# Kernel tuning notes

Measured on AMD Instinct MI355X. Metric: run time of the kernel, lower is better.

Reference implementation:

```python
import jax, jax.numpy as jnp
import numpy as np

DIAG = 4  # number of distinct power-of-2 diagonal bands; must divide H


def _diag_mask(H, L):
    # head h in group g = h // (H // DIAG) uses tril diagonal offset 2**g - 1.
    # True entries are MASKED (filled with -inf), except the last key column
    # which is always kept (cur_mask[:, -1] = 0 in the torch code).
    group = H // DIAG
    offs = 2 ** (jnp.arange(H) // group) - 1            # [H]
    rows = jnp.arange(L)[:, None]                        # [L,1] query index
    cols = jnp.arange(L)[None, :]                        # [1,L] key index
    mask = (cols <= rows + offs[:, None, None]) & (cols != L - 1)  # [H,L,L]
    return mask


def setup_inputs() -> dict:
    key = jax.random.key(0)
    kq, kk, kv = jax.random.split(key, 3)
    B, L, H, E = 4, 2048, 16, 64
    queries = jax.random.normal(kq, (B, L, H, E), dtype=jnp.float32)
    keys = jax.random.normal(kk, (B, L, H, E), dtype=jnp.float32)
    values = jax.random.normal(kv, (B, L, H, E), dtype=jnp.float32)
    return {"queries": queries, "keys": keys, "values": values}


def reference(queries, keys, values):
    B, L, H, E = queries.shape
    scale = 1.0 / np.sqrt(E).astype(np.float32)
    # [B,H,L,S]
    scores = jnp.einsum('blhe,bshe->bhls', queries, keys)
    mask = _diag_mask(H, L)                              # [H,L,L]
    scores = jnp.where(mask[None], -jnp.inf, scores)
    A = jax.nn.softmax(scale * scores, axis=-1)          # dropout inactive (eval)
    V = jnp.einsum('bhls,bshd->blhd', A, values)
    return V
```

## Files before the change

### kernel.cpp

```cpp
#include <hip/hip_runtime.h>
#include <stdint.h>

using f32x4  = __attribute__((ext_vector_type(4))) float;
using f32x16 = __attribute__((ext_vector_type(16))) float;
using s16x8  = __attribute__((ext_vector_type(8))) short;
using u16x4  = __attribute__((ext_vector_type(4))) unsigned short;
using u32x4  = __attribute__((ext_vector_type(4))) unsigned int;

typedef __attribute__((address_space(3))) unsigned int lds_u32;
typedef __attribute__((address_space(1))) unsigned int glb_u32;

__device__ __forceinline__ unsigned short f2bf(float f){
  union { float f; unsigned u; } x; x.f = f;
  return (unsigned short)((x.u + 0x7FFFu + ((x.u >> 16) & 1u)) >> 16);
}
__device__ __forceinline__ unsigned cvt_pk(float lo, float hi){
  unsigned r;
  asm("v_cvt_pk_bf16_f32 %0, %1, %2" : "=v"(r) : "v"(lo), "v"(hi));
  return r;
}
__device__ __forceinline__ void plswap(unsigned &a, unsigned &b){
  asm volatile("v_permlane32_swap_b32 %0, %1" : "+v"(a), "+v"(b));
}

#if __has_builtin(__builtin_amdgcn_exp2f)
#define EXP2F(x) __builtin_amdgcn_exp2f(x)
#else
#define EXP2F(x) exp2f(x)
#endif

#define MFMA16(A,B,C) __builtin_amdgcn_mfma_f32_16x16x32_bf16((A),(B),(C),0,0,0)
#define MFMA32(A,B,C) __builtin_amdgcn_mfma_f32_32x32x16_bf16((A),(B),(C),0,0,0)

constexpr int   L      = 2048;
constexpr int   H      = 16;
constexpr int   E      = 64;
constexpr int   HE     = 1024;
constexpr float SCALE  = 0.125f;
constexpr float QSCALE = 0.18033688011112042f;

__global__ __launch_bounds__(256)
void prep_kv(const float* __restrict__ Kg, const float* __restrict__ Vg,
             unsigned short* __restrict__ Ko, unsigned short* __restrict__ Vo){
  __shared__ __align__(16) unsigned short t8[4096];
  const int g0 = blockIdx.x;
  const int t  = threadIdx.x;
  if (g0 < 2048){
    const int gid = g0;
    const int jt = gid & 31, bh = gid >> 5;
    const int b = bh >> 4, h = bh & 15;
    const int key6 = t >> 2;
    const int p    = t & 3;
    const int kb = key6 >> 5, k31 = key6 & 31;
    const float* src = Kg + ((size_t)((b*2048 + jt*64 + key6)*16 + h) << 6) + p*16;
    const float4 v0 = *reinterpret_cast<const float4*>(src);
    const float4 v1 = *reinterpret_cast<const float4*>(src + 4);
    const float4 v2 = *reinterpret_cast<const float4*>(src + 8);
    const float4 v3 = *reinterpret_cast<const float4*>(src + 12);
    s16x8 f0, f1;
    f0[0]=(short)f2bf(v0.x); f0[1]=(short)f2bf(v0.y); f0[2]=(short)f2bf(v0.z); f0[3]=(short)f2bf(v0.w);
    f0[4]=(short)f2bf(v1.x); f0[5]=(short)f2bf(v1.y); f0[6]=(short)f2bf(v1.z); f0[7]=(short)f2bf(v1.w);
    f1[0]=(short)f2bf(v2.x); f1[1]=(short)f2bf(v2.y); f1[2]=(short)f2bf(v2.z); f1[3]=(short)f2bf(v2.w);
    f1[4]=(short)f2bf(v3.x); f1[5]=(short)f2bf(v3.y); f1[6]=(short)f2bf(v3.z); f1[7]=(short)f2bf(v3.w);
    const int slot0 = ((kb*4 + p)*2 + 0)*32 + k31;
    *reinterpret_cast<s16x8*>(&t8[slot0*8])      = f0;
    *reinterpret_cast<s16x8*>(&t8[(slot0+32)*8]) = f1;
    __syncthreads();
    unsigned short* dst = Ko + ((size_t)gid << 12) + t*16;
    *reinterpret_cast<s16x8*>(dst)     = *reinterpret_cast<const s16x8*>(&t8[t*16]);
    *reinterpret_cast<s16x8*>(dst + 8) = *reinterpret_cast<const s16x8*>(&t8[t*16 + 8]);
  } else {
    const int gid = g0 - 2048;
    const int jt = gid & 31, bh = gid >> 5;
    const int b = bh >> 4, h = bh & 15;
    const int key6 = t >> 2;
    const int p    = t & 3;
    const int kc = key6 >> 4, h2 = (key6 >> 3) & 1, kr = key6 & 7;
    const float* src = Vg + ((size_t)((b*2048 + jt*64 + key6)*16 + h) << 6) + p*16;
    float vv[16];
    #pragma unroll
    for (int q = 0; q < 4; ++q){
      const float4 v = *reinterpret_cast<const float4*>(src + q*4);
      vv[q*4+0]=v.x; vv[q*4+1]=v.y; vv[q*4+2]=v.z; vv[q*4+3]=v.w;
    }
    #pragma unroll
    for (int j = 0; j < 16; ++j){
      const int e  = p*16 + j;
      const int eb = e >> 5, e31 = e & 31;
      const int slot = ((eb*4 + kc)*2 + h2)*32 + e31;
      t8[slot*8 + kr] = f2bf(vv[j]);
    }
    __syncthreads();
    unsigned short* dst = Vo + ((size_t)gid << 12) + t*16;
    *reinterpret_cast<s16x8*>(dst)     = *reinterpret_cast<const s16x8*>(&t8[t*16]);
    *reinterpret_cast<s16x8*>(dst + 8) = *reinterpret_cast<const s16x8*>(&t8[t*16 + 8]);
  }
}

__global__ __launch_bounds__(512, 4)
void attn13(const float* __restrict__ Qg, const unsigned short* __restrict__ Kbg,
            const unsigned short* __restrict__ Vtg, float* __restrict__ Og)
{
  __shared__ __align__(16) unsigned short Kbuf[2][4096];
  __shared__ __align__(16) unsigned short Vbuf[2][4096];

  const int tid  = threadIdx.x;
  const int wave = tid >> 6;
  const int lane = tid & 63;
  const int c    = lane & 31;
  const int hi   = lane >> 5;

  const int gid = blockIdx.x;
  const int u   = gid >> 6;
  const int bh  = gid & 63;
  const int qb  = (u < 4) ? u : (11 - u);
  const int b = bh >> 4, h = bh & 15;
  const int off = (1 << (h >> 2)) - 1;

  const int    qrow0 = 256 * qb + wave * 32;
  const size_t fbase = (size_t)b * L * HE + (size_t)h * 64;
  const size_t tbase = (size_t)bh * 32;

  s16x8 qf[4];
  {
    const float* qp_ = Qg + fbase + (size_t)(qrow0 + c) * HE;
    #pragma unroll
    for (int ec = 0; ec < 4; ++ec){
      const float4 a  = *reinterpret_cast<const float4*>(qp_ + ec*16 + hi*8);
      const float4 b2 = *reinterpret_cast<const float4*>(qp_ + ec*16 + hi*8 + 4);
      s16x8 v;
      v[0]=(short)f2bf(a.x*QSCALE);  v[1]=(short)f2bf(a.y*QSCALE);
      v[2]=(short)f2bf(a.z*QSCALE);  v[3]=(short)f2bf(a.w*QSCALE);
      v[4]=(short)f2bf(b2.x*QSCALE); v[5]=(short)f2bf(b2.y*QSCALE);
      v[6]=(short)f2bf(b2.z*QSCALE); v[7]=(short)f2bf(b2.w*QSCALE);
      qf[ec] = v;
    }
  }

  s16x8 ones;
  #pragma unroll
  for (int j = 0; j < 8; ++j) ones[j] = (short)0x3F80;

  f32x16 acc0, acc1, accl;
  #pragma unroll
  for (int r = 0; r < 16; ++r){ acc0[r]=0.f; acc1[r]=0.f; accl[r]=0.f; }

  const int j0   = 4 * qb;
  const int qlim = qrow0 + c + off;

  auto STAGE = [&](int jt, int nb){
    const unsigned short* gk = Kbg + ((size_t)(tbase + jt) << 12) + (size_t)(wave*512 + lane*8);
    const unsigned short* gv = Vtg + ((size_t)(tbase + jt) << 12) + (size_t)(wave*512 + lane*8);
    __builtin_amdgcn_global_load_lds((const glb_u32*)gk,
        (lds_u32*)&Kbuf[nb][wave*512], 16, 0, 0);
    __builtin_amdgcn_global_load_lds((const glb_u32*)gv,
        (lds_u32*)&Vbuf[nb][wave*512], 16, 0, 0);
  };

  auto COMP = [&](int jt, int nb){
    const int s0 = jt * 64;
    if ((jt < 31) && (s0 + 63 <= qrow0 + off)) return;
    const unsigned short* KB = Kbuf[nb];
    const unsigned short* VB = Vbuf[nb];

    f32x16 S0, S1;
    #pragma unroll
    for (int r = 0; r < 16; ++r){ S0[r]=0.f; S1[r]=0.f; }
    __builtin_amdgcn_s_setprio(1);
    #pragma unroll
    for (int ec = 0; ec < 4; ++ec){
      const s16x8 k0 = *reinterpret_cast<const s16x8*>(&KB[(((0*4+ec)*2+hi)*32 + c)*8]);
      const s16x8 k1 = *reinterpret_cast<const s16x8*>(&KB[(((1*4+ec)*2+hi)*32 + c)*8]);
      S0 = MFMA32(k0, qf[ec], S0);
      S1 = MFMA32(k1, qf[ec], S1);
    }
    __builtin_amdgcn_s_setprio(0);

    if ((jt == 31) || (s0 <= qrow0 + 31 + off)){
      #pragma unroll
      for (int r = 0; r < 16; ++r){
        const int kg0 = s0 + (r&3) + 8*(r>>2) + 4*hi;
        const int kg1 = kg0 + 32;
        if (!((kg0 > qlim) || (kg0 == L-1))) S0[r] = -1e30f;
        if (!((kg1 > qlim) || (kg1 == L-1))) S1[r] = -1e30f;
      }
    }

    #pragma unroll
    for (int r = 0; r < 16; ++r){
      S0[r] = EXP2F(S0[r]);
      S1[r] = EXP2F(S1[r]);
    }

    __builtin_amdgcn_s_setprio(1);
    #define PV_STEP(Pv, kh, kcg) { \
      unsigned a0 = cvt_pk(Pv[8*(kh)+0], Pv[8*(kh)+1]); \
      unsigned a1 = cvt_pk(Pv[8*(kh)+2], Pv[8*(kh)+3]); \
      unsigned b0 = cvt_pk(Pv[8*(kh)+4], Pv[8*(kh)+5]); \
      unsigned b1 = cvt_pk(Pv[8*(kh)+6], Pv[8*(kh)+7]); \
      plswap(a0, b0); plswap(a1, b1); \
      u32x4 afu; afu[0]=a0; afu[1]=a1; afu[2]=b0; afu[3]=b1; \
      const s16x8 af = __builtin_bit_cast(s16x8, afu); \
      const s16x8 vf0 = *reinterpret_cast<const s16x8*>(&VB[(((0*4+(kcg))*2+hi)*32 + c)*8]); \
      const s16x8 vf1 = *reinterpret_cast<const s16x8*>(&VB[(((1*4+(kcg))*2+hi)*32 + c)*8]); \
      acc0 = MFMA32(af, vf0, acc0); \
      acc1 = MFMA32(af, vf1, acc1); \
      accl = MFMA32(af, ones, accl); \
    }
    PV_STEP(S0, 0, 0)
    PV_STEP(S0, 1, 1)
    PV_STEP(S1, 0, 2)
    PV_STEP(S1, 1, 3)
    #undef PV_STEP
    __builtin_amdgcn_s_setprio(0);
  };

  #define WAITBAR2 asm volatile("s_waitcnt vmcnt(2)\n\ts_barrier" ::: "memory")
  #define WAITBAR0 asm volatile("s_waitcnt vmcnt(0)\n\ts_barrier" ::: "memory")
  #define BARRIER  __builtin_amdgcn_s_barrier()

  STAGE(j0, 0);
  STAGE(j0 + 1, 1);

  for (int jt = j0; jt < 30; ++jt){
    WAITBAR2;
    COMP(jt, jt & 1);
    BARRIER;
    STAGE(jt + 2, jt & 1);
  }
  WAITBAR2;
  COMP(30, 0);
  WAITBAR0;
  COMP(31, 1);

  #undef WAITBAR2
  #undef WAITBAR0
  #undef BARRIER

  #pragma unroll
  for (int r = 0; r < 16; ++r){
    const int rowr = (r&3) + 8*(r>>2) + 4*hi;
    const float li = 1.0f / accl[r];
    float* op = Og + fbase + (size_t)(qrow0 + rowr) * HE;
    op[c]      = acc0[r] * li;
    op[32 + c] = acc1[r] * li;
  }
}

__global__ __launch_bounds__(512)
void attn_band(const float* __restrict__ Qg, const float* __restrict__ Kg,
               const float* __restrict__ Vg, float* __restrict__ Og)
{
  __shared__ __align__(16) unsigned short Ks[64*64];
  __shared__ __align__(16) unsigned short Vs[64*64];
  __shared__ __align__(16) unsigned short Ps[8][16*64];
  const int tid  = threadIdx.x;
  const int wave = tid >> 6;
  const int lane = tid & 63;
  const int lo16 = lane & 15;
  const int hi4  = lane >> 4;
  const int gid = blockIdx.x;
  const int qb  = gid & 15;
  const int bh  = gid >> 4;
  const int b   = bh >> 4;
  const int h   = bh & 15;
  const int off = (1 << (h >> 2)) - 1;
  const int    r0   = qb * 128;
  const size_t base = (size_t)b * L * HE + (size_t)h * 64;
  const int qrow0 = r0 + wave * 16;
  s16x8 qf[2];
  {
    const float* qp = Qg + base + (size_t)(qrow0 + lo16) * HE;
    #pragma unroll
    for (int ec = 0; ec < 2; ++ec){
      const int e0 = ec*32 + hi4*8;
      s16x8 v;
      #pragma unroll
      for (int j = 0; j < 8; ++j) v[j] = (short)f2bf(qp[e0 + j]);
      qf[ec] = v;
    }
  }
  f32x4 acc[4];
  #pragma unroll
  for (int et = 0; et < 4; ++et) acc[et] = f32x4{0.f,0.f,0.f,0.f};
  float m_run[4], l_run[4];
  #pragma unroll
  for (int i = 0; i < 4; ++i){ m_run[i] = -1e30f; l_run[i] = 0.f; }
  const int j0 = (r0 + off + 1) >> 6;
  for (int jt = j0; jt < 32; ++jt){
    const int s0 = jt * 64;
    __syncthreads();
    {
      const int f4    = tid & 15;
      const int rbase = tid >> 4;
      #pragma unroll
      for (int p = 0; p < 2; ++p){
        const int row = p*32 + rbase;
        const float4 vv = *reinterpret_cast<const float4*>(
            Kg + base + (size_t)(s0 + row) * HE + f4*4);
        u16x4 w; w[0]=f2bf(vv.x); w[1]=f2bf(vv.y); w[2]=f2bf(vv.z); w[3]=f2bf(vv.w);
        const int idx = row*64 + ((f4*4) ^ ((row & 7) << 3));
        *reinterpret_cast<u16x4*>(&Ks[idx]) = w;
      }
    }
    {
      const int kb = tid >> 5;
      const int e0 = (tid & 31) * 2;
      float2 cc[4];
      #pragma unroll
      for (int j = 0; j < 4; ++j)
        cc[j] = *reinterpret_cast<const float2*>(
            Vg + base + (size_t)(s0 + 4*kb + j) * HE + e0);
      #pragma unroll
      for (int i = 0; i < 2; ++i){
        const int e = e0 + i;
        u16x4 w;
        w[0] = f2bf(i ? cc[0].y : cc[0].x);
        w[1] = f2bf(i ? cc[1].y : cc[1].x);
        w[2] = f2bf(i ? cc[2].y : cc[2].x);
        w[3] = f2bf(i ? cc[3].y : cc[3].x);
        const int idx = e*64 + ((kb*4) ^ ((e & 7) << 3));
        *reinterpret_cast<u16x4*>(&Vs[idx]) = w;
      }
    }
    __syncthreads();
    if (jt < 31 && s0 + 63 <= qrow0 + off) continue;
    f32x4 S[4];
    #pragma unroll
    for (int kt = 0; kt < 4; ++kt){
      const int key = kt*16 + lo16;
      f32x4 z = {0.f,0.f,0.f,0.f};
      #pragma unroll
      for (int ec = 0; ec < 2; ++ec){
        const int e = ec*32 + hi4*8;
        const s16x8 kf = *reinterpret_cast<const s16x8*>(
            &Ks[key*64 + (e ^ ((key & 7) << 3))]);
        z = MFMA16(qf[ec], kf, z);
      }
      S[kt] = z;
    }
    #pragma unroll
    for (int kt = 0; kt < 4; ++kt){
      const int kg = s0 + kt*16 + lo16;
      #pragma unroll
      for (int i = 0; i < 4; ++i){
        const int qg2 = qrow0 + hi4*4 + i;
        const bool ok = (kg > qg2 + off) || (kg == L-1);
        S[kt][i] = ok ? S[kt][i]*SCALE : -1e30f;
      }
    }
    #pragma unroll
    for (int i = 0; i < 4; ++i){
      float t = fmaxf(fmaxf(S[0][i],S[1][i]), fmaxf(S[2][i],S[3][i]));
      t = fmaxf(t, __shfl_xor(t,1));
      t = fmaxf(t, __shfl_xor(t,2));
      t = fmaxf(t, __shfl_xor(t,4));
      t = fmaxf(t, __shfl_xor(t,8));
      const float mn = fmaxf(m_run[i], t);
      const float rs = __expf(m_run[i] - mn);
      m_run[i]  = mn;
      l_run[i] *= rs;
      acc[0][i] *= rs; acc[1][i] *= rs; acc[2][i] *= rs; acc[3][i] *= rs;
    }
    unsigned short* pwv = Ps[wave];
    float rsum[4] = {0.f,0.f,0.f,0.f};
    #pragma unroll
    for (int kt = 0; kt < 4; ++kt){
      #pragma unroll
      for (int i = 0; i < 4; ++i){
        const float p = __expf(S[kt][i] - m_run[i]);
        rsum[i] += p;
        const int qr  = hi4*4 + i;
        const int col = kt*16 + lo16;
        pwv[qr*64 + (col ^ ((qr & 7) << 3))] = f2bf(p);
      }
    }
    #pragma unroll
    for (int i = 0; i < 4; ++i){
      float t = rsum[i];
      t += __shfl_xor(t,1); t += __shfl_xor(t,2);
      t += __shfl_xor(t,4); t += __shfl_xor(t,8);
      l_run[i] += t;
    }
    #pragma unroll
    for (int kc = 0; kc < 2; ++kc){
      const int kk = kc*32 + hi4*8;
      const s16x8 pf = *reinterpret_cast<const s16x8*>(
          &pwv[lo16*64 + (kk ^ ((lo16 & 7) << 3))]);
      #pragma unroll
      for (int et = 0; et < 4; ++et){
        const int e = et*16 + lo16;
        const s16x8 vf = *reinterpret_cast<const s16x8*>(
            &Vs[e*64 + (kk ^ ((e & 7) << 3))]);
        acc[et] = MFMA16(pf, vf, acc[et]);
      }
    }
  }
  #pragma unroll
  for (int i = 0; i < 4; ++i){
    const float inv = 1.0f / l_run[i];
    const int   qg2 = qrow0 + hi4*4 + i;
    float* op = Og + base + (size_t)qg2 * HE;
    #pragma unroll
    for (int et = 0; et < 4; ++et)
      op[et*16 + lo16] = acc[et][i] * inv;
  }
}

extern "C" void kernel_launch(void* const* d_in, const int* in_sizes, int n_in,
                              void* d_out, int out_size, void* d_ws, size_t ws_size,
                              hipStream_t stream) {
  const float* Q = (const float*)d_in[0];
  const float* K = (const float*)d_in[1];
  const float* V = (const float*)d_in[2];
  float* O = (float*)d_out;

  const size_t kb_bytes = (size_t)64 * 32 * 4096 * 2;
  const size_t need     = kb_bytes * 2;
  if (ws_size >= need) {
    unsigned short* Kb = (unsigned short*)d_ws;
    unsigned short* Vt = (unsigned short*)((char*)d_ws + kb_bytes);
    prep_kv<<<dim3(4096), dim3(256), 0, stream>>>(K, V, Kb, Vt);
    attn13 <<<dim3(512),  dim3(512), 0, stream>>>(Q, Kb, Vt, O);
  } else {
    attn_band<<<dim3(1024), dim3(512), 0, stream>>>(Q, K, V, O);
  }
}
```

Before: 72.03 us.

## Split each block's KV range across two wave groups and reduce through LDS

The attention kernel grows to 1024 threads per block. The two groups of 8 waves each process half of the KV tiles for the same 256 query rows, using separate double-buffered LDS regions. Because the softmax uses unnormalized exp2 with no running max, the partial numerators and denominators simply add. They are combined through LDS in two phases before normalization and the store. This halves the serial tile loop per block, which targets the imbalance across query blocks. The cost is a larger LDS footprint, extra barriers, and a launch bound of (1024,4) that may squeeze registers.

After: 82.76 us. 1.15x slower.

```diff
diff --git a/kernel.cpp b/kernel.cpp
--- a/kernel.cpp
+++ b/kernel.cpp
@@ -97,15 +97,20 @@
   }
 }
 
-__global__ __launch_bounds__(512, 4)
-void attn13(const float* __restrict__ Qg, const unsigned short* __restrict__ Kbg,
+__global__ __launch_bounds__(1024, 4)
+void attn18(const float* __restrict__ Qg, const unsigned short* __restrict__ Kbg,
             const unsigned short* __restrict__ Vtg, float* __restrict__ Og)
 {
-  __shared__ __align__(16) unsigned short Kbuf[2][4096];
-  __shared__ __align__(16) unsigned short Vbuf[2][4096];
+  __shared__ __align__(16) unsigned char smem[65536];
+  unsigned short* KbL = (unsigned short*)(smem);
+  unsigned short* VbL = (unsigned short*)(smem + 16384);
+  unsigned short* KbU = (unsigned short*)(smem + 32768);
+  unsigned short* VbU = (unsigned short*)(smem + 49152);
 
   const int tid  = threadIdx.x;
   const int wave = tid >> 6;
+  const int grp  = wave >> 3;
+  const int g    = wave & 7;
   const int lane = tid & 63;
   const int c    = lane & 31;
   const int hi   = lane >> 5;
@@ -117,9 +122,12 @@
   const int b = bh >> 4, h = bh & 15;
   const int off = (1 << (h >> 2)) - 1;
 
-  const int    qrow0 = 256 * qb + wave * 32;
+  const int    qrow0 = 256 * qb + g * 32;
   const size_t fbase = (size_t)b * L * HE + (size_t)h * 64;
   const size_t tbase = (size_t)bh * 32;
+
+  unsigned short* Kmy = grp ? KbU : KbL;
+  unsigned short* Vmy = grp ? VbU : VbL;
 
   s16x8 qf[4];
   {
@@ -145,23 +153,25 @@
   #pragma unroll
   for (int r = 0; r < 16; ++r){ acc0[r]=0.f; acc1[r]=0.f; accl[r]=0.f; }
 
-  const int j0   = 4 * qb;
-  const int qlim = qrow0 + c + off;
-
-  auto STAGE = [&](int jt, int nb){
-    const unsigned short* gk = Kbg + ((size_t)(tbase + jt) << 12) + (size_t)(wave*512 + lane*8);
-    const unsigned short* gv = Vtg + ((size_t)(tbase + jt) << 12) + (size_t)(wave*512 + lane*8);
+  const int niter  = 16 - 2*qb;
+  const int tbase0 = grp ? (16 + 2*qb) : (4*qb);
+  const int qlim   = qrow0 + c + off;
+
+  auto STAGE = [&](int tl, int nb){
+    const unsigned short* gk = Kbg + ((size_t)(tbase + tl) << 12) + (size_t)(g*512 + lane*8);
+    const unsigned short* gv = Vtg + ((size_t)(tbase + tl) << 12) + (size_t)(g*512 + lane*8);
     __builtin_amdgcn_global_load_lds((const glb_u32*)gk,
-        (lds_u32*)&Kbuf[nb][wave*512], 16, 0, 0);
+        (lds_u32*)(Kmy + nb*4096 + g*512), 16, 0, 0);
     __builtin_amdgcn_global_load_lds((const glb_u32*)gv,
-        (lds_u32*)&Vbuf[nb][wave*512], 16, 0, 0);
+        (lds_u32*)(Vmy + nb*4096 + g*512), 16, 0, 0);
   };
 
-  auto COMP = [&](int jt, int nb){
-    const int s0 = jt * 64;
-    if ((jt < 31) && (s0 + 63 <= qrow0 + off)) return;
-    const unsigned short* KB = Kbuf[nb];
-    const unsigned short* VB = Vbuf[nb];
+  auto COMP = [&](int tl, int nb){
+    const int s0 = tl * 64;
+    const bool last = (tl == 31);
+    if (!last && (s0 + 63 <= qrow0 + off)) return;
+    const unsigned short* KB = Kmy + nb*4096;
+    const unsigned short* VB = Vmy + nb*4096;
 
     f32x16 S0, S1;
     #pragma unroll
@@ -176,7 +186,7 @@
     }
     __builtin_amdgcn_s_setprio(0);
 
-    if ((jt == 31) || (s0 <= qrow0 + 31 + off)){
+    if (last || (s0 <= qrow0 + 31 + off)){
       #pragma unroll
       for (int r = 0; r < 16; ++r){
         const int kg0 = s0 + (r&3) + 8*(r>>2) + 4*hi;
@@ -219,31 +229,54 @@
   #define WAITBAR0 asm volatile("s_waitcnt vmcnt(0)\n\ts_barrier" ::: "memory")
   #define BARRIER  __builtin_amdgcn_s_barrier()
 
-  STAGE(j0, 0);
-  STAGE(j0 + 1, 1);
-
-  for (int jt = j0; jt < 30; ++jt){
+  STAGE(tbase0 + 0, 0);
+  STAGE(tbase0 + 1, 1);
+
+  for (int i = 0; i + 2 < niter; ++i){
     WAITBAR2;
-    COMP(jt, jt & 1);
+    COMP(tbase0 + i, i & 1);
     BARRIER;
-    STAGE(jt + 2, jt & 1);
+    STAGE(tbase0 + i + 2, i & 1);
   }
   WAITBAR2;
-  COMP(30, 0);
+  COMP(tbase0 + niter - 2, 0);
   WAITBAR0;
-  COMP(31, 1);
+  COMP(tbase0 + niter - 1, 1);
 
   #undef WAITBAR2
   #undef WAITBAR0
   #undef BARRIER
 
-  #pragma unroll
-  for (int r = 0; r < 16; ++r){
-    const int rowr = (r&3) + 8*(r>>2) + 4*hi;
-    const float li = 1.0f / accl[r];
-    float* op = Og + fbase + (size_t)(qrow0 + rowr) * HE;
-    op[c]      = acc0[r] * li;
-    op[32 + c] = acc1[r] * li;
+  __syncthreads();
+  float* accArea = (float*)smem;
+  float* lArea   = (float*)(smem + 4*64*33*4);
+  #pragma unroll
+  for (int phase = 0; phase < 2; ++phase){
+    const int gl = phase*4;
+    if (grp == 1 && g >= gl && g < gl+4){
+      float* A = accArea + (g-gl)*(64*33) + lane*33;
+      #pragma unroll
+      for (int r = 0; r < 16; ++r){ A[r] = acc0[r]; A[16+r] = acc1[r]; }
+      if (c == 0){
+        float* Lp = lArea + (g-gl)*32 + hi*16;
+        #pragma unroll
+        for (int r = 0; r < 16; ++r) Lp[r] = accl[r];
+      }
+    }
+    __syncthreads();
+    if (grp == 0 && g >= gl && g < gl+4){
+      const float* A  = accArea + (g-gl)*(64*33) + lane*33;
+      const float* Lp = lArea + (g-gl)*32 + hi*16;
+      #pragma unroll
+      for (int r = 0; r < 16; ++r){
+        const float li = 1.0f / (accl[r] + Lp[r]);
+        const int rowr = (r&3) + 8*(r>>2) + 4*hi;
+        float* op = Og + fbase + (size_t)(qrow0 + rowr) * HE;
+        op[c]      = (acc0[r] + A[r])    * li;
+        op[32 + c] = (acc1[r] + A[16+r]) * li;
+      }
+    }
+    __syncthreads();
   }
 }
 
@@ -421,7 +454,7 @@
     unsigned short* Kb = (unsigned short*)d_ws;
     unsigned short* Vt = (unsigned short*)((char*)d_ws + kb_bytes);
     prep_kv<<<dim3(4096), dim3(256), 0, stream>>>(K, V, Kb, Vt);
-    attn13 <<<dim3(512),  dim3(512), 0, stream>>>(Q, Kb, Vt, O);
+    attn18 <<<dim3(512),  dim3(1024), 0, stream>>>(Q, Kb, Vt, O);
   } else {
     attn_band<<<dim3(1024), dim3(512), 0, stream>>>(Q, K, V, O);
   }
```
